# Kernel tuning notes

Measured on AMD Instinct MI355X. Metric: run time of the kernel, lower is better.

## Reference

```python
import jax, jax.numpy as jnp
import numpy as np

QWEN_H = 2048
SNN_H = 512


def setup_inputs() -> dict:
    key = jax.random.key(0)
    k0, k1, k2, k3, k4 = jax.random.split(key, 5)
    hidden_states = jax.random.normal(k0, (4, 2048, QWEN_H), dtype=jnp.float32)
    # nn.Linear weights stored as [out, in]
    w_down = jax.random.normal(k1, (SNN_H, QWEN_H), dtype=jnp.float32) / np.sqrt(QWEN_H)
    w_up = jax.random.normal(k2, (QWEN_H, SNN_H), dtype=jnp.float32) / np.sqrt(SNN_H)
    w1 = jax.random.normal(k3, (SNN_H, SNN_H), dtype=jnp.float32) / np.sqrt(SNN_H)
    w2 = jax.random.normal(k4, (SNN_H, SNN_H), dtype=jnp.float32) / np.sqrt(SNN_H)
    residual_scale = jnp.float32(0.1)
    return {"hidden_states": hidden_states, "w_down": w_down, "w_up": w_up,
            "w1": w1, "w2": w2, "residual_scale": residual_scale}


def reference(hidden_states, w_down, w_up, w1, w2, residual_scale):
    # Faithful math of SNNMiddleLayer.forward. The spike pulse encode ->
    # SpikeFP32Linear (fp32 accumulation) -> pulse decode path is a lossless
    # FP32 spike encoding of an ordinary bias-free linear layer, so the
    # per-timestep loop computes exactly out_t = w2 @ (w1 @ proj_down(x_t)),
    # which we express as fused batched GEMMs over all timesteps.
    residual = hidden_states
    x = jnp.einsum('bsq,hq->bsh', hidden_states, w_down)   # proj_down
    h = jnp.einsum('bsh,oh->bso', x, w1)                   # snn_linear1
    o = jnp.einsum('bso,po->bsp', h, w2)                   # snn_linear2
    out = jnp.einsum('bsp,qp->bsq', o, w_up)               # proj_up
    return residual + residual_scale * out
```

## Files before the change

### kernel.cpp

```cpp
#include <hip/hip_runtime.h>
#include <hip/hip_bf16.h>
#include <stdint.h>

using bf16 = __hip_bfloat16;
typedef __attribute__((ext_vector_type(8))) short bf16x8;
typedef __attribute__((ext_vector_type(4))) float f32x4;

__device__ __forceinline__ void async_load16(const void* g, void* l) {
    __builtin_amdgcn_global_load_lds(
        (__attribute__((address_space(1))) const void*)g,
        (__attribute__((address_space(3))) void*)l,
        16, 0, 0);
}

__device__ __forceinline__ void cvt_block_2048(const float* __restrict__ src,
                                               bf16* __restrict__ dst, int relblk) {
    int i = (relblk * 256 + (int)threadIdx.x) * 8;
    float4 f0 = *(const float4*)(src + i);
    float4 f1 = *(const float4*)(src + i + 4);
    union { bf16 h[8]; uint4 u; } o;
    o.h[0] = __float2bfloat16(f0.x); o.h[1] = __float2bfloat16(f0.y);
    o.h[2] = __float2bfloat16(f0.z); o.h[3] = __float2bfloat16(f0.w);
    o.h[4] = __float2bfloat16(f1.x); o.h[5] = __float2bfloat16(f1.y);
    o.h[6] = __float2bfloat16(f1.z); o.h[7] = __float2bfloat16(f1.w);
    *(uint4*)(dst + i) = o.u;
}

__global__ __launch_bounds__(256) void prep_w(
    const float* __restrict__ w1, bf16* __restrict__ w1b,
    const float* __restrict__ wup, bf16* __restrict__ wub,
    const float* __restrict__ wd, bf16* __restrict__ wdt,
    const float* __restrict__ w2, bf16* __restrict__ w2t) {
    __shared__ bf16 sh[32][33];
    int b = blockIdx.x;
    if (b < 128)       { cvt_block_2048(w1, w1b, b); return; }
    if (b < 640)       { cvt_block_2048(wup, wub, b - 128); return; }
    const float* src; bf16* dst; int R, C, tile, ntx;
    if (b < 1664) { src = wd; dst = wdt; R = 512; C = 2048; tile = b - 640; ntx = 64; }
    else          { src = w2; dst = w2t; R = 512; C = 512;  tile = b - 1664; ntx = 16; }
    const int bx = (tile % ntx) * 32, by = (tile / ntx) * 32;
    const int lx = threadIdx.x & 31;
    const int ly4 = ((int)threadIdx.x >> 5) * 4;
#pragma unroll
    for (int r = 0; r < 4; ++r)
        sh[ly4 + r][lx] = __float2bfloat16(src[(size_t)(by + ly4 + r) * C + bx + lx]);
    __syncthreads();
#pragma unroll
    for (int r = 0; r < 4; ++r)
        dst[(size_t)(bx + ly4 + r) * R + by + lx] = sh[lx][ly4 + r];
}

template<int BN, int NW>
__device__ __forceinline__ void stage_tiles(
    const bf16* __restrict__ A, const bf16* __restrict__ B,
    size_t bm, size_t bn, int K, int k0,
    bf16* __restrict__ As, bf16* __restrict__ Bs, int wave, int lane)
{
    const int srow = lane >> 3;
    const int scol = (lane & 7) ^ srow;
    constexpr int NCH = (128 + BN) / 8;
#pragma unroll
    for (int c = 0; c < NCH / NW; ++c) {
        const int cc = wave + c * NW;
        if (cc < 16) {
            const int rb = cc * 8;
            async_load16(A + (bm + rb + srow) * (size_t)K + k0 + scol * 8,
                         &As[rb * 64]);
        } else {
            const int rb = (cc - 16) * 8;
            async_load16(B + (bn + rb + srow) * (size_t)K + k0 + scol * 8,
                         &Bs[rb * 64]);
        }
    }
}

template<int BN, int EPI, int KT, int NW>
__device__ __forceinline__ void gemm_core(
    const bf16* __restrict__ A, const bf16* __restrict__ B,
    bf16* __restrict__ Cb, float* __restrict__ Cf,
    const float* __restrict__ Res, const float* __restrict__ sp,
    int N, int K, int bxi, int byi, bf16* smem)
{
    constexpr int BM = 128;
    constexpr int BK = 64;
    constexpr int WN = NW / 2;
    constexpr int NJ = 2;
    constexpr int BUF = (BM + BN) * BK;
    static_assert(BN == WN * 32, "wave tile is 64x32");
    static_assert(NW == 4 || NW == 8, "NW");
    static_assert(EPI == 0 || (NW == 8 && KT == 512), "EPI path: 8 waves, KT=512");

    const int tid  = threadIdx.x;
    const int wave = tid >> 6;
    const int lane = tid & 63;
    const int wm = wave / WN, wn = wave % WN;
    const size_t bm = (size_t)bxi * BM;
    const size_t bn = (size_t)byi * BN;

    f32x4 acc[4][NJ];
#pragma unroll
    for (int i = 0; i < 4; ++i)
#pragma unroll
        for (int j = 0; j < NJ; ++j)
            acc[i][j] = (f32x4){0.f, 0.f, 0.f, 0.f};

    float4 res_pre[EPI ? 8 : 1];
    const int r16 = lane >> 3;
    const int cbb = (lane & 7) * 4;

    auto compute_tile = [&](const bf16* Ap, const bf16* Bp) {
#pragma unroll
        for (int kk = 0; kk < 2; ++kk) {
            const int c8 = kk * 4 + (lane >> 4);
            bf16x8 af[4], bfr[NJ];
#pragma unroll
            for (int i = 0; i < 4; ++i) {
                const int r = wm * 64 + i * 16 + (lane & 15);
                af[i] = *(const bf16x8*)&Ap[(size_t)(r * 8 + (c8 ^ (r & 7))) * 8];
            }
#pragma unroll
            for (int j = 0; j < NJ; ++j) {
                const int r = wn * 32 + j * 16 + (lane & 15);
                bfr[j] = *(const bf16x8*)&Bp[(size_t)(r * 8 + (c8 ^ (r & 7))) * 8];
            }
#pragma unroll
            for (int i = 0; i < 4; ++i)
#pragma unroll
                for (int j = 0; j < NJ; ++j)
                    acc[i][j] = __builtin_amdgcn_mfma_f32_16x16x32_bf16(af[i], bfr[j], acc[i][j], 0, 0, 0);
        }
    };

    stage_tiles<BN, NW>(A, B, bm, bn, K, 0, smem, smem + BM * BK, wave, lane);
    __syncthreads();

    if constexpr (KT > 0) {
#pragma unroll
        for (int it = 0; it < KT / BK; ++it) {
            const int cur = it & 1;
            if (it + 1 < KT / BK) {
                bf16* nb = smem + (cur ^ 1) * BUF;
                stage_tiles<BN, NW>(A, B, bm, bn, KT, (it + 1) * BK, nb, nb + BM * BK, wave, lane);
            }
            if constexpr (EPI) {
                const int i = it >> 1, rh = it & 1;
                size_t row = bm + wm * 64 + i * 16 + rh * 8 + r16;
                size_t col = bn + wn * 32 + cbb;
                res_pre[it] = *(const float4*)&Res[row * (size_t)N + col];
            }
            const bf16* Ap = smem + cur * BUF;
            compute_tile(Ap, Ap + BM * BK);
            __syncthreads();
        }
    } else {
        int cur = 0;
        for (int k0 = 0; k0 < K; k0 += BK) {
            if (k0 + BK < K) {
                bf16* nb = smem + (cur ^ 1) * BUF;
                stage_tiles<BN, NW>(A, B, bm, bn, K, k0 + BK, nb, nb + BM * BK, wave, lane);
            }
            const bf16* Ap = smem + cur * BUF;
            compute_tile(Ap, Ap + BM * BK);
            __syncthreads();
            cur ^= 1;
        }
    }

    const int col_l = lane & 15;
    const int row_l = (lane >> 4) * 4;
    if (EPI == 0) {
#pragma unroll
        for (int i = 0; i < 4; ++i)
#pragma unroll
            for (int j = 0; j < NJ; ++j)
#pragma unroll
                for (int r = 0; r < 4; ++r) {
                    size_t row = bm + wm * 64 + i * 16 + row_l + r;
                    size_t col = bn + wn * 32 + j * 16 + col_l;
                    Cb[row * (size_t)N + col] = __float2bfloat16(acc[i][j][r]);
                }
    } else {
        const float s = *sp;
        float* lds_f = (float*)smem + wave * (16 * 36);
#pragma unroll
        for (int i = 0; i < 4; ++i) {
#pragma unroll
            for (int j = 0; j < NJ; ++j)
#pragma unroll
                for (int r = 0; r < 4; ++r)
                    lds_f[(row_l + r) * 36 + j * 16 + col_l] = acc[i][j][r];
#pragma unroll
            for (int rh = 0; rh < 2; ++rh) {
                const int rr = rh * 8 + r16;
                float4 v = *(float4*)&lds_f[rr * 36 + cbb];
                size_t row = bm + wm * 64 + i * 16 + rr;
                size_t col = bn + wn * 32 + cbb;
                size_t idx = row * (size_t)N + col;
                float4 rv = res_pre[i * 2 + rh];
                float4 o;
                o.x = rv.x + s * v.x; o.y = rv.y + s * v.y;
                o.z = rv.z + s * v.z; o.w = rv.w + s * v.w;
                *(float4*)&Cf[idx] = o;
            }
        }
    }
}

template<int BN, int EPI, int KT, int NW>
__global__ __launch_bounds__(NW * 64) void gemm_bf16(
    const bf16* __restrict__ A, const bf16* __restrict__ B,
    bf16* __restrict__ Cb, float* __restrict__ Cf,
    const float* __restrict__ Res, const float* __restrict__ sp, int N, int K) {
    __shared__ __align__(16) bf16 smem[(128 + BN) * 64 * 2];
    const int nx = gridDim.x;
    const int flat = blockIdx.y * nx + blockIdx.x;
    const int chunk = (nx * gridDim.y) >> 3;
    const int swz = (flat & 7) * chunk + (flat >> 3);
    gemm_core<BN, EPI, KT, NW>(A, B, Cb, Cf, Res, sp, N, K,
                               swz / nx, swz % nx, smem);
}

__global__ __launch_bounds__(256) void ru_cvt(
    const bf16* __restrict__ A0, const bf16* __restrict__ B0, bf16* __restrict__ C0,
    const bf16* __restrict__ A1, const bf16* __restrict__ B1, bf16* __restrict__ C1,
    const float* __restrict__ hs, bf16* __restrict__ hsb) {
    __shared__ __align__(16) bf16 smem[(128 + 64) * 64 * 2];
    int b = blockIdx.x;
    if (b < 128)
        gemm_core<64, 0, 0, 4>(A0, B0, C0, nullptr, nullptr, nullptr, 2048, 512,
                               b / 32, b % 32, smem);
    else if (b < 256) {
        int bb = b - 128;
        gemm_core<64, 0, 0, 4>(A1, B1, C1, nullptr, nullptr, nullptr, 512, 512,
                               bb / 8, bb % 8, smem);
    } else
        cvt_block_2048(hs, hsb, b - 256);
}

extern "C" void kernel_launch(void* const* d_in, const int* in_sizes, int n_in,
                              void* d_out, int out_size, void* d_ws, size_t ws_size,
                              hipStream_t stream) {
    const float* hs     = (const float*)d_in[0];
    const float* w_down = (const float*)d_in[1];
    const float* w_up   = (const float*)d_in[2];
    const float* w1     = (const float*)d_in[3];
    const float* w2     = (const float*)d_in[4];
    const float* rs     = (const float*)d_in[5];

    char* ws = (char*)d_ws;
    bf16* hs_b  = (bf16*)(ws + 0);
    bf16* x_b   = (bf16*)(ws + 33554432);
    bf16* w1_b  = (bf16*)(ws + 41943040);
    bf16* wu_b  = (bf16*)(ws + 42467328);
    bf16* wdt_b = (bf16*)(ws + 44564480);
    bf16* w2t_b = (bf16*)(ws + 46661632);
    bf16* Rm    = (bf16*)(ws + 47185920);
    bf16* Um    = (bf16*)(ws + 49283072);

    prep_w<<<dim3(1920), dim3(256), 0, stream>>>(w1, w1_b, w_up, wu_b, w_down, wdt_b, w2, w2t_b);
    ru_cvt<<<dim3(256 + 8192), dim3(256), 0, stream>>>(w1_b, wdt_b, Rm, wu_b, w2t_b, Um, hs, hs_b);
    gemm_bf16<128, 0, 0, 8><<<dim3(4, 64), dim3(512), 0, stream>>>(hs_b, Rm, x_b, nullptr,
                                                                   nullptr, nullptr, 512, 2048);
    gemm_bf16<128, 1, 512, 8><<<dim3(16, 64), dim3(512), 0, stream>>>(x_b, Um, nullptr, (float*)d_out,
                                                                      hs, rs, 2048, 512);
}
```

Before: 182.6 us.

## Fuse fp32-to-bf16 conversion of hidden states into the down-projection GEMM

The separate pass that converts the 32 MB fp32 hidden states to bf16 in workspace is removed. A new x_gemm kernel loads fp32 A tiles into registers, converts them, and writes them to swizzled LDS, with B staged asynchronously and double-buffered. This drops a full write and re-read of the bf16 copy. In exchange the GEMM reads twice as many A bytes, uses 256 threads instead of 512, and depends on register-staged prefetch to hide the load latency.

Result: slower. 191.7 us (+5.0%).

```diff
diff --git a/kernel.cpp b/kernel.cpp
--- a/kernel.cpp
+++ b/kernel.cpp
@@ -220,21 +220,136 @@
                                swz / nx, swz % nx, smem);
 }
 
-__global__ __launch_bounds__(256) void ru_cvt(
+__global__ __launch_bounds__(256) void x_gemm(
+    const float* __restrict__ A32, const bf16* __restrict__ B,
+    bf16* __restrict__ Cb, int N, int K)
+{
+    constexpr int BM = 128, BN = 128, BK = 64;
+    constexpr int BUF = (BM + BN) * BK;
+    __shared__ __align__(16) bf16 smem[BUF * 2];
+
+    const int nx = gridDim.x;
+    const int flat = blockIdx.y * nx + blockIdx.x;
+    const int chunk = (nx * gridDim.y) >> 3;
+    const int swz = (flat & 7) * chunk + (flat >> 3);
+    const int bxi = swz / nx, byi = swz % nx;
+    const size_t bm = (size_t)bxi * BM;
+    const size_t bn = (size_t)byi * BN;
+
+    const int tid = threadIdx.x, wave = tid >> 6, lane = tid & 63;
+    const int wm = wave >> 1, wn = wave & 1;
+
+    f32x4 acc[4][4];
+#pragma unroll
+    for (int i = 0; i < 4; ++i)
+#pragma unroll
+        for (int j = 0; j < 4; ++j)
+            acc[i][j] = (f32x4){0.f, 0.f, 0.f, 0.f};
+
+    float4 av[4][2];
+
+    auto loadA = [&](int k0) {
+#pragma unroll
+        for (int u = 0; u < 4; ++u) {
+            const int unit = tid + u * 256;
+            const int r = unit >> 3, c8 = unit & 7;
+            const float* g = A32 + (bm + r) * (size_t)K + k0 + c8 * 8;
+            av[u][0] = *(const float4*)g;
+            av[u][1] = *(const float4*)(g + 4);
+        }
+    };
+    auto writeA = [&](bf16* As) {
+#pragma unroll
+        for (int u = 0; u < 4; ++u) {
+            const int unit = tid + u * 256;
+            const int r = unit >> 3, c8 = unit & 7;
+            const int su = (r >> 3) * 64 + (r & 7) * 8 + (c8 ^ (r & 7));
+            union { bf16 h[8]; uint4 q; } o;
+            o.h[0] = __float2bfloat16(av[u][0].x); o.h[1] = __float2bfloat16(av[u][0].y);
+            o.h[2] = __float2bfloat16(av[u][0].z); o.h[3] = __float2bfloat16(av[u][0].w);
+            o.h[4] = __float2bfloat16(av[u][1].x); o.h[5] = __float2bfloat16(av[u][1].y);
+            o.h[6] = __float2bfloat16(av[u][1].z); o.h[7] = __float2bfloat16(av[u][1].w);
+            *(uint4*)&As[(size_t)su * 8] = o.q;
+        }
+    };
+    auto stageB = [&](bf16* Bs, int k0) {
+        const int srow = lane >> 3;
+        const int scol = (lane & 7) ^ srow;
+#pragma unroll
+        for (int c = 0; c < 4; ++c) {
+            const int rb = (wave + c * 4) * 8;
+            async_load16(B + (bn + rb + srow) * (size_t)K + k0 + scol * 8,
+                         &Bs[rb * 64]);
+        }
+    };
+    auto compute = [&](const bf16* Ap, const bf16* Bp) {
+#pragma unroll
+        for (int kk = 0; kk < 2; ++kk) {
+            const int c8 = kk * 4 + (lane >> 4);
+            bf16x8 af[4], bfr[4];
+#pragma unroll
+            for (int i = 0; i < 4; ++i) {
+                const int r = wm * 64 + i * 16 + (lane & 15);
+                af[i] = *(const bf16x8*)&Ap[(size_t)(r * 8 + (c8 ^ (r & 7))) * 8];
+            }
+#pragma unroll
+            for (int j = 0; j < 4; ++j) {
+                const int r = wn * 64 + j * 16 + (lane & 15);
+                bfr[j] = *(const bf16x8*)&Bp[(size_t)(r * 8 + (c8 ^ (r & 7))) * 8];
+            }
+#pragma unroll
+            for (int i = 0; i < 4; ++i)
+#pragma unroll
+                for (int j = 0; j < 4; ++j)
+                    acc[i][j] = __builtin_amdgcn_mfma_f32_16x16x32_bf16(af[i], bfr[j], acc[i][j], 0, 0, 0);
+        }
+    };
+
+    loadA(0);
+    writeA(smem);
+    stageB(smem + BM * BK, 0);
+    __syncthreads();
+
+    int cur = 0;
+    for (int k0 = 0; k0 < K; k0 += BK) {
+        const bool more = (k0 + BK) < K;
+        if (more) {
+            loadA(k0 + BK);
+            stageB(smem + (cur ^ 1) * BUF + BM * BK, k0 + BK);
+        }
+        compute(smem + cur * BUF, smem + cur * BUF + BM * BK);
+        if (more) writeA(smem + (cur ^ 1) * BUF);
+        __syncthreads();
+        cur ^= 1;
+    }
+
+    const int col_l = lane & 15;
+    const int row_l = (lane >> 4) * 4;
+#pragma unroll
+    for (int i = 0; i < 4; ++i)
+#pragma unroll
+        for (int j = 0; j < 4; ++j)
+#pragma unroll
+            for (int r = 0; r < 4; ++r) {
+                size_t row = bm + wm * 64 + i * 16 + row_l + r;
+                size_t col = bn + wn * 64 + j * 16 + col_l;
+                Cb[row * (size_t)N + col] = __float2bfloat16(acc[i][j][r]);
+            }
+}
+
+__global__ __launch_bounds__(256) void ru(
     const bf16* __restrict__ A0, const bf16* __restrict__ B0, bf16* __restrict__ C0,
-    const bf16* __restrict__ A1, const bf16* __restrict__ B1, bf16* __restrict__ C1,
-    const float* __restrict__ hs, bf16* __restrict__ hsb) {
+    const bf16* __restrict__ A1, const bf16* __restrict__ B1, bf16* __restrict__ C1) {
     __shared__ __align__(16) bf16 smem[(128 + 64) * 64 * 2];
     int b = blockIdx.x;
     if (b < 128)
         gemm_core<64, 0, 0, 4>(A0, B0, C0, nullptr, nullptr, nullptr, 2048, 512,
                                b / 32, b % 32, smem);
-    else if (b < 256) {
+    else {
         int bb = b - 128;
         gemm_core<64, 0, 0, 4>(A1, B1, C1, nullptr, nullptr, nullptr, 512, 512,
                                bb / 8, bb % 8, smem);
-    } else
-        cvt_block_2048(hs, hsb, b - 256);
+    }
 }
 
 extern "C" void kernel_launch(void* const* d_in, const int* in_sizes, int n_in,
@@ -248,7 +363,6 @@
     const float* rs     = (const float*)d_in[5];
 
     char* ws = (char*)d_ws;
-    bf16* hs_b  = (bf16*)(ws + 0);
     bf16* x_b   = (bf16*)(ws + 33554432);
     bf16* w1_b  = (bf16*)(ws + 41943040);
     bf16* wu_b  = (bf16*)(ws + 42467328);
@@ -258,9 +372,8 @@
     bf16* Um    = (bf16*)(ws + 49283072);
 
     prep_w<<<dim3(1920), dim3(256), 0, stream>>>(w1, w1_b, w_up, wu_b, w_down, wdt_b, w2, w2t_b);
-    ru_cvt<<<dim3(256 + 8192), dim3(256), 0, stream>>>(w1_b, wdt_b, Rm, wu_b, w2t_b, Um, hs, hs_b);
-    gemm_bf16<128, 0, 0, 8><<<dim3(4, 64), dim3(512), 0, stream>>>(hs_b, Rm, x_b, nullptr,
-                                                                   nullptr, nullptr, 512, 2048);
+    ru<<<dim3(256), dim3(256), 0, stream>>>(w1_b, wdt_b, Rm, wu_b, w2t_b, Um);
+    x_gemm<<<dim3(4, 64), dim3(256), 0, stream>>>(hs, Rm, x_b, 512, 2048);
     gemm_bf16<128, 1, 512, 8><<<dim3(16, 64), dim3(512), 0, stream>>>(x_b, Um, nullptr, (float*)d_out,
                                                                       hs, rs, 2048, 512);
 }
```
